# Performance work log

Hardware: AMD Instinct MI355X
Metric: run time of the kernel (lower is better)

Reference implementation:

```python
import jax, jax.numpy as jnp
import numpy as np

N = 10000      # nodes
E = 320000     # edges (avg degree 32)
D = 512        # input features
H = 2048       # dim_hidden hard-coded in module
C = 40         # num_classes


def setup_inputs() -> dict:
    key = jax.random.key(0)
    k = jax.random.split(key, 4)
    x = jax.random.normal(k[0], (N, D), dtype=jnp.float32)
    edge_index = jax.random.randint(k[1], (2, E), 0, N)
    W1 = jax.random.normal(k[2], (D, H), dtype=jnp.float32) * (1.0 / np.sqrt(D))
    b1 = jnp.zeros((H,), jnp.float32)
    W2 = jax.random.normal(k[3], (H, C), dtype=jnp.float32) * (1.0 / np.sqrt(H))
    b2 = jnp.zeros((C,), jnp.float32)
    return {"x": x, "edge_index": edge_index, "W1": W1, "b1": b1, "W2": W2, "b2": b2}


def _sym_norm(edge_index, n):
    # GCN symmetric normalization with self-loops: deg includes the self loop.
    src, dst = edge_index[0], edge_index[1]
    deg = jnp.zeros((n,), jnp.float32).at[dst].add(1.0) + 1.0
    dinv = jax.lax.rsqrt(deg)
    return src, dst, dinv


def _propagate(h, src, dst, dinv):
    # out[i] = sum_{j->i} dinv[j]*dinv[i]*h[j]  +  dinv[i]^2 * h[i] (self loop)
    coef = (dinv[src] * dinv[dst])[:, None]            # [E,1]
    agg = jax.ops.segment_sum(h[src] * coef, dst, num_segments=h.shape[0])
    return agg + h * (dinv * dinv)[:, None]


def _gcn_conv(x, W, b, src, dst, dinv):
    # A_hat (X W) == (A_hat X) W; aggregate in the smaller feature dim.
    if W.shape[0] <= W.shape[1]:
        return _propagate(x, src, dst, dinv) @ W + b
    return _propagate(x @ W, src, dst, dinv) + b


def reference(x, edge_index, W1, b1, W2, b2):
    src, dst, dinv = _sym_norm(edge_index, x.shape[0])
    h = jax.nn.relu(_gcn_conv(x, W1, b1, src, dst, dinv))
    return _gcn_conv(h, W2, b2, src, dst, dinv)
```

## Files before the change

kernel.cpp:

```cpp
#include <hip/hip_runtime.h>
#include <stdint.h>

#define N_NODES 10000
#define N_EDGES 320000
#define D_IN    512
#define D_HID   2048
#define N_CLS   40
#define MP2     10240
#define HSTR    136

typedef float f32x4  __attribute__((ext_vector_type(4)));
typedef short bf16x8 __attribute__((ext_vector_type(8)));
typedef unsigned short us8 __attribute__((ext_vector_type(8)));

__device__ inline unsigned short f2bf(float f){
  unsigned int u = __float_as_uint(f);
  u += 0x7fffu + ((u >> 16) & 1u);
  return (unsigned short)(u >> 16);
}

__device__ inline float bf2f(unsigned short h){
  return __uint_as_float(((unsigned int)h) << 16);
}

__device__ inline void gl_lds16(const void* g, void* l){
  __builtin_amdgcn_global_load_lds((const __attribute__((address_space(1))) void*)g,
                                   (__attribute__((address_space(3))) void*)l, 16, 0, 0);
}

__global__ void k_prep0(const float* __restrict__ x, unsigned short* __restrict__ Xb,
                        const int* __restrict__ ei, int* __restrict__ deg){
  if (blockIdx.x < 2500){
    int idx = blockIdx.x*256 + threadIdx.x;
    const f32x4* x4 = (const f32x4*)x;
    f32x4 a = x4[idx*2], b = x4[idx*2+1];
    us8 o;
    o[0]=f2bf(a.x); o[1]=f2bf(a.y); o[2]=f2bf(a.z); o[3]=f2bf(a.w);
    o[4]=f2bf(b.x); o[5]=f2bf(b.y); o[6]=f2bf(b.z); o[7]=f2bf(b.w);
    *(us8*)(Xb + (size_t)idx*8) = o;
  } else {
    int e = (blockIdx.x - 2500)*256 + threadIdx.x;
    if (e < N_EDGES) atomicAdd(&deg[ei[N_EDGES + e]], 1);
  }
}

__global__ void k_scan(const int* __restrict__ deg, int* __restrict__ cursor,
                       float* __restrict__ dinv){
  __shared__ int sdeg[N_NODES];
  __shared__ int sums[1024];
  const int t = threadIdx.x;
  for (int j = t; j < N_NODES; j += 1024){
    int v = deg[j];
    sdeg[j] = v;
    dinv[j] = rsqrtf((float)v + 1.0f);
  }
  __syncthreads();
  const int CH = 10;
  int base = t*CH;
  int local[CH]; int s = 0;
  for (int j = 0; j < CH; j++){
    int v = (base + j < N_NODES) ? sdeg[base + j] : 0;
    local[j] = s; s += v;
  }
  sums[t] = s;
  __syncthreads();
  for (int off = 1; off < 1024; off <<= 1){
    int v = (t >= off) ? sums[t - off] : 0;
    __syncthreads();
    sums[t] += v;
    __syncthreads();
  }
  int pre = (t > 0) ? sums[t-1] : 0;
  for (int j = 0; j < CH; j++){
    int idx = base + j;
    if (idx < N_NODES) sdeg[idx] = pre + local[j];
  }
  __syncthreads();
  for (int j = t; j < N_NODES; j += 1024) cursor[j] = sdeg[j];
}

__global__ void k_fill(const int* __restrict__ ei, int* __restrict__ cursor, int* __restrict__ csr_src){
  int e = blockIdx.x*256 + threadIdx.x;
  if (e < N_EDGES){
    int s = ei[e], d = ei[N_EDGES + e];
    int pos = atomicAdd(&cursor[d], 1);
    csr_src[pos] = s;
  }
}

__global__ __launch_bounds__(256) void k_gjoint(const unsigned short* __restrict__ Xb,
                          const int* __restrict__ csr_src,
                          const int* __restrict__ cursor, const int* __restrict__ deg,
                          const float* __restrict__ dinv, unsigned short* __restrict__ Pb,
                          const float* __restrict__ W1, unsigned short* __restrict__ Wt1,
                          const float* __restrict__ W2, unsigned short* __restrict__ Wt2){
  __shared__ float tile[32][33];
  if (blockIdx.x < 2500){
    const int w    = threadIdx.x >> 6;
    const int lane = threadIdx.x & 63;
    const int i    = blockIdx.x*4 + w;
    const float di = dinv[i];
    float acc[8];
    us8 xi = *(const us8*)(Xb + (size_t)i*D_IN + lane*8);
    const float dii = di*di;
    #pragma unroll
    for (int r = 0; r < 8; r++) acc[r] = dii * bf2f(xi[r]);
    const int cnt = deg[i];
    const int start = cursor[i] - cnt;
    const unsigned short* Xl = Xb + lane*8;
    for (int c0 = 0; c0 < cnt; c0 += 64){
      int m = cnt - c0; if (m > 64) m = 64;
      int s = 0; float cf = 0.0f;
      if (lane < m){ s = csr_src[start + c0 + lane]; cf = dinv[s]*di; }
      int j = 0;
      for (; j + 8 <= m; j += 8){
        int   s0 = __shfl(s, j),   s1 = __shfl(s, j+1), s2 = __shfl(s, j+2), s3 = __shfl(s, j+3);
        int   s4 = __shfl(s, j+4), s5 = __shfl(s, j+5), s6 = __shfl(s, j+6), s7 = __shfl(s, j+7);
        float c0f = __shfl(cf, j),   c1f = __shfl(cf, j+1), c2f = __shfl(cf, j+2), c3f = __shfl(cf, j+3);
        float c4f = __shfl(cf, j+4), c5f = __shfl(cf, j+5), c6f = __shfl(cf, j+6), c7f = __shfl(cf, j+7);
        us8 x0 = *(const us8*)(Xl + (size_t)s0*D_IN);
        us8 x1 = *(const us8*)(Xl + (size_t)s1*D_IN);
        us8 x2 = *(const us8*)(Xl + (size_t)s2*D_IN);
        us8 x3 = *(const us8*)(Xl + (size_t)s3*D_IN);
        us8 x4 = *(const us8*)(Xl + (size_t)s4*D_IN);
        us8 x5 = *(const us8*)(Xl + (size_t)s5*D_IN);
        us8 x6 = *(const us8*)(Xl + (size_t)s6*D_IN);
        us8 x7 = *(const us8*)(Xl + (size_t)s7*D_IN);
        #pragma unroll
        for (int r = 0; r < 8; r++) acc[r] += c0f * bf2f(x0[r]);
        #pragma unroll
        for (int r = 0; r < 8; r++) acc[r] += c1f * bf2f(x1[r]);
        #pragma unroll
        for (int r = 0; r < 8; r++) acc[r] += c2f * bf2f(x2[r]);
        #pragma unroll
        for (int r = 0; r < 8; r++) acc[r] += c3f * bf2f(x3[r]);
        #pragma unroll
        for (int r = 0; r < 8; r++) acc[r] += c4f * bf2f(x4[r]);
        #pragma unroll
        for (int r = 0; r < 8; r++) acc[r] += c5f * bf2f(x5[r]);
        #pragma unroll
        for (int r = 0; r < 8; r++) acc[r] += c6f * bf2f(x6[r]);
        #pragma unroll
        for (int r = 0; r < 8; r++) acc[r] += c7f * bf2f(x7[r]);
      }
      for (; j < m; j++){
        int   sj = __shfl(s, j);
        float cj = __shfl(cf, j);
        us8 xr = *(const us8*)(Xl + (size_t)sj*D_IN);
        #pragma unroll
        for (int r = 0; r < 8; r++) acc[r] += cj * bf2f(xr[r]);
      }
    }
    us8 o;
    #pragma unroll
    for (int r = 0; r < 8; r++) o[r] = f2bf(acc[r]);
    *(us8*)(Pb + (size_t)i*D_IN + lane*8) = o;
  } else if (blockIdx.x < 2500 + 1024){
    const int bb = blockIdx.x - 2500;
    const int n0 = (bb & 63)*32, k0 = (bb >> 6)*32;
    const int tx = threadIdx.x & 31, ty = threadIdx.x >> 5;
    for (int i = 0; i < 32; i += 8)
      tile[ty+i][tx] = W1[(size_t)(k0+ty+i)*D_HID + n0+tx];
    __syncthreads();
    for (int i = 0; i < 32; i += 8)
      Wt1[(size_t)(n0+ty+i)*D_IN + k0+tx] = f2bf(tile[tx][ty+i]);
  } else {
    int idx = (blockIdx.x - 3524)*256 + threadIdx.x;
    if (idx < 48*D_HID){
      int n = idx >> 11, k = idx & (D_HID-1);
      Wt2[idx] = (n < N_CLS) ? f2bf(W2[k*N_CLS + n]) : (unsigned short)0;
    }
  }
}

__global__ __launch_bounds__(512, 4) void k_gemm1f(const unsigned short* __restrict__ Pb,
                                                   const unsigned short* __restrict__ Wt1,
                                                   const float* __restrict__ b1,
                                                   const unsigned short* __restrict__ Wt2,
                                                   float* __restrict__ Gp){
  __shared__ short smem[256*HSTR];
  short* Hs = smem;
  const int t    = threadIdx.x;
  const int lane = t & 63;
  const int wid  = t >> 6;
  const int wm   = (wid >> 1)*64;
  const int wn   = (wid & 1)*64;
  const int m0   = blockIdx.y*256, n0 = blockIdx.x*128;
  const int arow = t >> 2;
  const int akof = ((t & 3) ^ ((t >> 3) & 3))*8;
  const int fr   = lane & 15;
  const int q    = lane >> 4;
  const int sq8  = (q ^ ((fr >> 1) & 3))*8;

  const unsigned short* ApA = Pb  + (size_t)(m0 +       arow)*D_IN + akof;
  const unsigned short* ApB = Pb  + (size_t)(m0 + 128 + arow)*D_IN + akof;
  const unsigned short* BpA = Wt1 + (size_t)(n0 +       arow)*D_IN + akof;

  f32x4 acc[4][4] = {};
  {
    gl_lds16(ApA, smem + t*8);
    gl_lds16(ApB, smem + 4096 + t*8);
    gl_lds16(BpA, smem + 8192 + t*8);
  }
  #pragma unroll
  for (int ks = 0; ks < 16; ks++){
    if (ks < 15){
      short* buf = smem + ((ks+1)&1)*12288;
      const int kb = (ks+1)*32;
      gl_lds16(ApA + kb, buf + t*8);
      gl_lds16(ApB + kb, buf + 4096 + t*8);
      gl_lds16(BpA + kb, buf + 8192 + t*8);
      asm volatile("" ::: "memory");
      __builtin_amdgcn_s_waitcnt(0x0F73);
    } else {
      asm volatile("" ::: "memory");
      __builtin_amdgcn_s_waitcnt(0x0F70);
    }
    __builtin_amdgcn_s_barrier();
    asm volatile("" ::: "memory");
    const short* As = smem + (ks&1)*12288;
    const short* Bs = As + 8192;
    bf16x8 a[4], b[4];
    #pragma unroll
    for (int i = 0; i < 4; i++) a[i] = *(const bf16x8*)(As + (wm + i*16 + fr)*32 + sq8);
    #pragma unroll
    for (int j = 0; j < 4; j++) b[j] = *(const bf16x8*)(Bs + (wn + j*16 + fr)*32 + sq8);
    #pragma unroll
    for (int i = 0; i < 4; i++)
      #pragma unroll
      for (int j = 0; j < 4; j++)
        acc[i][j] = __builtin_amdgcn_mfma_f32_16x16x32_bf16(a[i], b[j], acc[i][j], 0, 0, 0);
    asm volatile("" ::: "memory");
    __builtin_amdgcn_s_barrier();
    asm volatile("" ::: "memory");
  }
  #pragma unroll
  for (int j = 0; j < 4; j++){
    int col = wn + j*16 + fr;
    float bias = b1[n0 + col];
    #pragma unroll
    for (int i = 0; i < 4; i++){
      int rbase = wm + i*16 + q*4;
      f32x4 v = acc[i][j];
      #pragma unroll
      for (int r = 0; r < 4; r++){
        float h = fmaxf(v[r] + bias, 0.0f);
        Hs[(rbase + r)*HSTR + col] = (short)f2bf(h);
      }
    }
  }
  __syncthreads();
  f32x4 acc2[2][3] = {};
  for (int ks = 0; ks < 4; ks++){
    bf16x8 a2[2];
    #pragma unroll
    for (int i2 = 0; i2 < 2; i2++)
      a2[i2] = *(const bf16x8*)(Hs + (wid*32 + i2*16 + fr)*HSTR + ks*32 + q*8);
    #pragma unroll
    for (int j2 = 0; j2 < 3; j2++){
      bf16x8 b2 = *(const bf16x8*)(Wt2 + (size_t)(j2*16 + fr)*D_HID + n0 + ks*32 + q*8);
      #pragma unroll
      for (int i2 = 0; i2 < 2; i2++)
        acc2[i2][j2] = __builtin_amdgcn_mfma_f32_16x16x32_bf16(a2[i2], b2, acc2[i2][j2], 0, 0, 0);
    }
  }
  float* Gpp = Gp + (size_t)blockIdx.x*N_NODES*N_CLS;
  #pragma unroll
  for (int j2 = 0; j2 < 3; j2++){
    int col = j2*16 + fr;
    if (col < N_CLS){
      #pragma unroll
      for (int i2 = 0; i2 < 2; i2++){
        int rbase = m0 + wid*32 + i2*16 + q*4;
        f32x4 v = acc2[i2][j2];
        #pragma unroll
        for (int r = 0; r < 4; r++){
          int row = rbase + r;
          if (row < N_NODES)
            Gpp[(size_t)row*N_CLS + col] = v[r];
        }
      }
    }
  }
}

__global__ void k_reduceG(const float* __restrict__ Gp, float* __restrict__ G){
  int idx = blockIdx.x*256 + threadIdx.x;
  if (idx < N_NODES*N_CLS){
    float s = 0.0f;
    #pragma unroll
    for (int p = 0; p < 16; p++)
      s += Gp[(size_t)p*N_NODES*N_CLS + idx];
    G[idx] = s;
  }
}

__global__ void k_gather2(const float* __restrict__ G, const int* __restrict__ csr_src,
                          const int* __restrict__ cursor, const int* __restrict__ deg,
                          const float* __restrict__ dinv, const float* __restrict__ b2,
                          float* __restrict__ out){
  __shared__ int   ssrc[64];
  __shared__ float scoef[64];
  const int i = blockIdx.x;
  const int t = threadIdx.x;
  const float di = dinv[i];
  const int cnt = deg[i];
  const int start = cursor[i] - cnt;
  float acc = 0.0f;
  if (t < N_CLS) acc = di*di * G[i*N_CLS + t];
  for (int c0 = 0; c0 < cnt; c0 += 64){
    int m = cnt - c0; if (m > 64) m = 64;
    if (t < m){
      int s = csr_src[start + c0 + t];
      ssrc[t] = s; scoef[t] = dinv[s]*di;
    }
    __syncthreads();
    if (t < N_CLS)
      for (int j = 0; j < m; j++)
        acc += scoef[j] * G[ssrc[j]*N_CLS + t];
    __syncthreads();
  }
  if (t < N_CLS) out[i*N_CLS + t] = acc + b2[t];
}

extern "C" void kernel_launch(void* const* d_in, const int* in_sizes, int n_in,
                              void* d_out, int out_size, void* d_ws, size_t ws_size,
                              hipStream_t stream){
  const float* x  = (const float*)d_in[0];
  const int*   ei = (const int*)d_in[1];
  const float* W1 = (const float*)d_in[2];
  const float* b1 = (const float*)d_in[3];
  const float* W2 = (const float*)d_in[4];
  const float* b2 = (const float*)d_in[5];
  float* out = (float*)d_out;

  char* ws = (char*)d_ws;
  size_t off = 0;
  auto alloc = [&](size_t bytes) -> void* {
    void* p = ws + off; off += (bytes + 255) & ~(size_t)255; return p;
  };
  int*   deg     = (int*)alloc((size_t)N_NODES*4);
  float* dinv    = (float*)alloc((size_t)N_NODES*4);
  int*   cursor  = (int*)alloc((size_t)N_NODES*4);
  int*   csr     = (int*)alloc((size_t)N_EDGES*4);
  unsigned short* Xb  = (unsigned short*)alloc((size_t)N_NODES*D_IN*2);
  unsigned short* Pb  = (unsigned short*)alloc((size_t)MP2*D_IN*2);
  unsigned short* Wt1 = (unsigned short*)alloc((size_t)D_HID*D_IN*2);
  unsigned short* Wt2 = (unsigned short*)alloc((size_t)48*D_HID*2);
  float* G  = (float*)alloc((size_t)N_NODES*N_CLS*4);
  float* Gp = (float*)alloc((size_t)16*N_NODES*N_CLS*4);

  hipMemsetAsync(deg, 0, (size_t)N_NODES*4, stream);

  k_prep0<<<2500 + 1250, 256, 0, stream>>>(x, Xb, ei, deg);
  k_scan<<<1, 1024, 0, stream>>>(deg, cursor, dinv);
  k_fill<<<(N_EDGES+255)/256, 256, 0, stream>>>(ei, cursor, csr);
  k_gjoint<<<2500 + 1024 + 384, 256, 0, stream>>>(Xb, csr, cursor, deg, dinv, Pb,
                                                  W1, Wt1, W2, Wt2);
  k_gemm1f<<<dim3(D_HID/128, MP2/256), 512, 0, stream>>>(Pb, Wt1, b1, Wt2, Gp);
  k_reduceG<<<(N_NODES*N_CLS + 255)/256, 256, 0, stream>>>(Gp, G);
  k_gather2<<<N_NODES, 64, 0, stream>>>(G, csr, cursor, deg, dinv, b2, out);
}
```

Baseline: 215.3 us.

## Split first-layer gather into column slices with four nodes per wavefront

The first-layer aggregation is restructured so each wavefront handles four nodes, with 16 lanes per node. The feature dimension is split into four 128-column slices across block groups, so all nodes' 128-column slices are gathered together, which may improve L2 locality of the gathered rows. Edge indices are fetched 16 at a time per node group, and the loop runs to the maximum degree among the four nodes, with padded entries carrying zero coefficients. The trade-offs are wasted iterations from degree imbalance within a wavefront and each edge list being read four times.

```diff
diff --git a/kernel.cpp b/kernel.cpp
--- a/kernel.cpp
+++ b/kernel.cpp
@@ -98,26 +98,35 @@
   if (blockIdx.x < 2500){
     const int w    = threadIdx.x >> 6;
     const int lane = threadIdx.x & 63;
-    const int i    = blockIdx.x*4 + w;
+    const int g    = lane >> 4;
+    const int sub  = lane & 15;
+    const int sl   = blockIdx.x / 625;
+    const int nb   = blockIdx.x - sl*625;
+    const int i    = nb*16 + w*4 + g;
+    const int col0 = sl*128;
     const float di = dinv[i];
+    const unsigned short* Xl = Xb + col0 + sub*8;
     float acc[8];
-    us8 xi = *(const us8*)(Xb + (size_t)i*D_IN + lane*8);
+    us8 xi = *(const us8*)(Xl + (size_t)i*D_IN);
     const float dii = di*di;
     #pragma unroll
     for (int r = 0; r < 8; r++) acc[r] = dii * bf2f(xi[r]);
     const int cnt = deg[i];
     const int start = cursor[i] - cnt;
-    const unsigned short* Xl = Xb + lane*8;
-    for (int c0 = 0; c0 < cnt; c0 += 64){
-      int m = cnt - c0; if (m > 64) m = 64;
-      int s = 0; float cf = 0.0f;
-      if (lane < m){ s = csr_src[start + c0 + lane]; cf = dinv[s]*di; }
+    int mc = cnt;
+    mc = max(mc, __shfl_xor(mc, 16));
+    mc = max(mc, __shfl_xor(mc, 32));
+    for (int c0 = 0; c0 < mc; c0 += 16){
+      int s = i; float cf = 0.0f;
+      if (sub < cnt - c0){ s = csr_src[start + c0 + sub]; cf = dinv[s]*di; }
+      int jm = mc - c0; if (jm > 16) jm = 16;
+      const int lb = g*16;
       int j = 0;
-      for (; j + 8 <= m; j += 8){
-        int   s0 = __shfl(s, j),   s1 = __shfl(s, j+1), s2 = __shfl(s, j+2), s3 = __shfl(s, j+3);
-        int   s4 = __shfl(s, j+4), s5 = __shfl(s, j+5), s6 = __shfl(s, j+6), s7 = __shfl(s, j+7);
-        float c0f = __shfl(cf, j),   c1f = __shfl(cf, j+1), c2f = __shfl(cf, j+2), c3f = __shfl(cf, j+3);
-        float c4f = __shfl(cf, j+4), c5f = __shfl(cf, j+5), c6f = __shfl(cf, j+6), c7f = __shfl(cf, j+7);
+      for (; j + 8 <= jm; j += 8){
+        int   s0 = __shfl(s, lb+j),   s1 = __shfl(s, lb+j+1), s2 = __shfl(s, lb+j+2), s3 = __shfl(s, lb+j+3);
+        int   s4 = __shfl(s, lb+j+4), s5 = __shfl(s, lb+j+5), s6 = __shfl(s, lb+j+6), s7 = __shfl(s, lb+j+7);
+        float c0f = __shfl(cf, lb+j),   c1f = __shfl(cf, lb+j+1), c2f = __shfl(cf, lb+j+2), c3f = __shfl(cf, lb+j+3);
+        float c4f = __shfl(cf, lb+j+4), c5f = __shfl(cf, lb+j+5), c6f = __shfl(cf, lb+j+6), c7f = __shfl(cf, lb+j+7);
         us8 x0 = *(const us8*)(Xl + (size_t)s0*D_IN);
         us8 x1 = *(const us8*)(Xl + (size_t)s1*D_IN);
         us8 x2 = *(const us8*)(Xl + (size_t)s2*D_IN);
@@ -143,9 +152,9 @@
         #pragma unroll
         for (int r = 0; r < 8; r++) acc[r] += c7f * bf2f(x7[r]);
       }
-      for (; j < m; j++){
-        int   sj = __shfl(s, j);
-        float cj = __shfl(cf, j);
+      for (; j < jm; j++){
+        int   sj = __shfl(s, lb+j);
+        float cj = __shfl(cf, lb+j);
         us8 xr = *(const us8*)(Xl + (size_t)sj*D_IN);
         #pragma unroll
         for (int r = 0; r < 8; r++) acc[r] += cj * bf2f(xr[r]);
@@ -154,7 +163,7 @@
     us8 o;
     #pragma unroll
     for (int r = 0; r < 8; r++) o[r] = f2bf(acc[r]);
-    *(us8*)(Pb + (size_t)i*D_IN + lane*8) = o;
+    *(us8*)(Pb + (size_t)i*D_IN + col0 + sub*8) = o;
   } else if (blockIdx.x < 2500 + 1024){
     const int bb = blockIdx.x - 2500;
     const int n0 = (bb & 63)*32, k0 = (bb >> 6)*32;
```

After: 209.2 us. -2.8%, faster.
